# Performance work log

Hardware: AMD Instinct MI355X
Metric: run time of the kernel (lower is better)

The kernel has to match this reference:

```python
import jax, jax.numpy as jnp
import numpy as np

NP_, NA_ = 50000, 20000
D_IN, D_HID, D_OUT = 128, 128, 64
E_W, E_C, E_R = 250000, 500000, 250000


def setup_inputs() -> dict:
    key = jax.random.key(0)
    ks = jax.random.split(key, 14)
    s_in = 1.0 / np.sqrt(D_IN)
    s_h = 1.0 / np.sqrt(D_HID)
    return {
        "x_paper": jax.random.normal(ks[0], (NP_, D_IN), jnp.float32),
        "x_author": jax.random.normal(ks[1], (NA_, D_IN), jnp.float32),
        "Wl1": jax.random.normal(ks[2], (3, D_HID, D_IN), jnp.float32) * s_in,
        "bl1": jax.random.normal(ks[3], (3, D_HID), jnp.float32) * 0.01,
        "Wr1": jax.random.normal(ks[4], (3, D_HID, D_IN), jnp.float32) * s_in,
        "Wl2": jax.random.normal(ks[5], (3, D_OUT, D_HID), jnp.float32) * s_h,
        "bl2": jax.random.normal(ks[6], (3, D_OUT), jnp.float32) * 0.01,
        "Wr2": jax.random.normal(ks[7], (3, D_OUT, D_HID), jnp.float32) * s_h,
        "writes_src": jax.random.randint(ks[8], (E_W,), 0, NA_),
        "writes_dst": jax.random.randint(ks[9], (E_W,), 0, NP_),
        "cites_src": jax.random.randint(ks[10], (E_C,), 0, NP_),
        "cites_dst": jax.random.randint(ks[11], (E_C,), 0, NP_),
        "rev_src": jax.random.randint(ks[12], (E_R,), 0, NP_),
        "rev_dst": jax.random.randint(ks[13], (E_R,), 0, NA_),
    }


def _sage(x_src, x_dst, src, dst, Wl, bl, Wr, n_dst):
    # PyG SAGEConv(aggr='mean'): lin_l(mean_j x_src[j]) + lin_r(x_dst)
    agg = jax.ops.segment_sum(x_src[src], dst, num_segments=n_dst)
    cnt = jax.ops.segment_sum(jnp.ones_like(dst, dtype=x_src.dtype), dst,
                              num_segments=n_dst)
    agg = agg / jnp.maximum(cnt, 1.0)[:, None]  # degree-0 nodes -> 0 (PyG scatter-mean)
    return agg @ Wl.T + bl + x_dst @ Wr.T


def reference(x_paper, x_author, Wl1, bl1, Wr1, Wl2, bl2, Wr2,
              writes_src, writes_dst, cites_src, cites_dst, rev_src, rev_dst):
    def hetero_layer(xp, xa, Wl, bl, Wr):
        # HeteroConv(aggr='mean'): average per-relation outputs per dst node type
        op = 0.5 * (_sage(xa, xp, writes_src, writes_dst, Wl[0], bl[0], Wr[0], NP_)
                    + _sage(xp, xp, cites_src, cites_dst, Wl[1], bl[1], Wr[1], NP_))
        oa = _sage(xp, xa, rev_src, rev_dst, Wl[2], bl[2], Wr[2], NA_)
        return op, oa

    hp, ha = hetero_layer(x_paper, x_author, Wl1, bl1, Wr1)
    hp, ha = jax.nn.relu(hp), jax.nn.relu(ha)  # norm_type='none', dropout eval-mode
    hp, _ = hetero_layer(hp, ha, Wl2, bl2, Wr2)
    return hp  # logits for category='paper', [NP_, D_OUT]
```

## Files before the change

### kernel.cpp

```cpp
#include <hip/hip_runtime.h>

#define NP 50000
#define NA 20000
#define E_W 250000
#define E_C 500000
#define E_R 250000
#define E_TOT (E_W + E_C + E_R)
#define CAP 48
#define RBLK 8192
#define NSEG 123
#define NCHP 782
#define NCHA 313
#define NBIN (NCHP + NCHA)

typedef __attribute__((ext_vector_type(8))) short short8;
typedef __attribute__((ext_vector_type(4))) float floatx4;
typedef __attribute__((ext_vector_type(2))) float floatx2;

__device__ __forceinline__ unsigned short f2bf(float f) {
    unsigned u = __float_as_uint(f);
    return (unsigned short)((u + 0x7FFFu + ((u >> 16) & 1u)) >> 16);
}
__device__ __forceinline__ float bflo(unsigned v) { return __uint_as_float(v << 16); }
__device__ __forceinline__ float bfhi(unsigned v) { return __uint_as_float(v & 0xFFFF0000u); }

__device__ __forceinline__ int frag_off(int NT, int j, int n, int k) {
    int t = n >> 4, ln = n & 15;
    int kb = k >> 5, q = (k >> 3) & 3, r = k & 7;
    return (((j * NT + t) * 4 + kb) * 64 + q * 16 + ln) * 8 + r;
}

__device__ __forceinline__ void prep_body(
    int idx,
    const float* __restrict__ xp, const float* __restrict__ xa,
    const float* __restrict__ Wl1, const float* __restrict__ Wr1,
    const float* __restrict__ Wl2, const float* __restrict__ Wr2,
    const float* __restrict__ bl1, const float* __restrict__ bl2,
    unsigned short* __restrict__ xpb, unsigned short* __restrict__ xab,
    unsigned* __restrict__ xp8, unsigned* __restrict__ xa8,
    unsigned short* __restrict__ Wp1, unsigned short* __restrict__ Wa1,
    unsigned short* __restrict__ Wt2, unsigned short* __restrict__ Wr2s,
    float* __restrict__ bias_p1, float* __restrict__ bias_a1,
    float* __restrict__ bias_p2) {
    const int n4p = NP * 32, n4a = NA * 32;
    if (idx < n4p + n4a) {
        const float* s; unsigned short* d; unsigned* d8; int i = idx;
        if (i < n4p) { s = xp; d = xpb; d8 = xp8; }
        else { s = xa; d = xab; d8 = xa8; i -= n4p; }
        float4 v = ((const float4*)s)[i];
        ushort4 u;
        u.x = f2bf(v.x); u.y = f2bf(v.y); u.z = f2bf(v.z); u.w = f2bf(v.w);
        ((ushort4*)d)[i] = u;
        int w = __builtin_amdgcn_cvt_pk_fp8_f32(v.x, v.y, 0, false);
        w = __builtin_amdgcn_cvt_pk_fp8_f32(v.z, v.w, w, true);
        d8[i] = (unsigned)w;
        return;
    }
    int j = idx - (n4p + n4a);
    if (j < 49152) {
        int jj = j >> 14, rem = j & 16383, n = rem >> 7, k = rem & 127;
        float v = (jj == 0)   ? 0.5f * Wl1[rem]
                  : (jj == 1) ? 0.5f * Wl1[16384 + rem]
                              : 0.5f * (Wr1[rem] + Wr1[16384 + rem]);
        Wp1[frag_off(8, jj, n, k)] = f2bf(v);
    } else if (j < 81920) {
        int i2 = j - 49152;
        int jj = i2 >> 14, rem = i2 & 16383, n = rem >> 7, k = rem & 127;
        float v = (jj == 0) ? Wl1[2 * 16384 + rem] : Wr1[2 * 16384 + rem];
        Wa1[frag_off(8, jj, n, k)] = f2bf(v);
    } else if (j < 98304) {
        int i2 = j - 81920;
        int jj = i2 >> 13, rem = i2 & 8191, n = rem >> 7, k = rem & 127;
        float v = 0.5f * Wl2[jj * 8192 + rem];
        Wt2[frag_off(4, jj, n, k)] = f2bf(v);
    } else if (j < 106496) {
        int i2 = j - 98304;
        int n = i2 >> 7, k = i2 & 127;
        float v = 0.5f * (Wr2[i2] + Wr2[8192 + i2]);
        Wr2s[frag_off(4, 0, n, k)] = f2bf(v);
    } else if (j < 106496 + 320) {
        int b = j - 106496;
        if (b < 128) bias_p1[b] = 0.5f * (bl1[b] + bl1[128 + b]);
        else if (b < 256) bias_a1[b - 128] = bl1[256 + b - 128];
        else bias_p2[b - 256] = 0.5f * (bl2[b - 256] + bl2[64 + b - 256]);
    }
}

__device__ __forceinline__ void edge_bin(
    int e, const int* __restrict__ w_src, const int* __restrict__ w_dst,
    const int* __restrict__ c_src, const int* __restrict__ c_dst,
    const int* __restrict__ r_src, const int* __restrict__ r_dst,
    int& bin, int& sub, int& src) {
    bool isC = (e >= E_W) & (e < E_W + E_C);
    bool isR = e >= E_W + E_C;
    const int* db = isR ? r_dst : (isC ? c_dst : w_dst);
    const int* sb = isR ? r_src : (isC ? c_src : w_src);
    int idx = e - (isC ? E_W : 0) - (isR ? (E_W + E_C) : 0);
    int d = db[idx];
    src = sb[idx];
    if (isR) { bin = NCHP + (d >> 6); sub = d & 63; }
    else { bin = d >> 6; sub = (d & 63) + (isC ? 64 : 0); }
}

__device__ __forceinline__ void route_body(
    int bid, const int* __restrict__ w_src, const int* __restrict__ w_dst,
    const int* __restrict__ c_src, const int* __restrict__ c_dst,
    const int* __restrict__ r_src, const int* __restrict__ r_dst,
    unsigned* __restrict__ seg, unsigned* __restrict__ segmeta,
    int* cnt_s, int* base_s, int* cur_s) {
    int tid = threadIdx.x, lane = tid & 63;
    for (int k = tid; k < NBIN; k += 256) cnt_s[k] = 0;
    __syncthreads();
#pragma unroll 4
    for (int u = 0; u < 32; ++u) {
        int e = bid * RBLK + u * 256 + tid;
        if (e < E_TOT) {
            int bin, sub, src;
            edge_bin(e, w_src, w_dst, c_src, c_dst, r_src, r_dst, bin, sub, src);
            atomicAdd(&cnt_s[bin], 1);
        }
    }
    __syncthreads();
    if (tid < 64) {
        int v[18], tot = 0;
#pragma unroll
        for (int q = 0; q < 18; ++q) {
            int k = tid * 18 + q;
            v[q] = (k < NBIN) ? cnt_s[k] : 0;
            tot += v[q];
        }
        int sc = tot;
#pragma unroll
        for (int ofs = 1; ofs < 64; ofs <<= 1) {
            int t = __shfl_up(sc, ofs, 64);
            if (lane >= ofs) sc += t;
        }
        int run = sc - tot;
#pragma unroll
        for (int q = 0; q < 18; ++q) {
            int k = tid * 18 + q;
            if (k < NBIN) { base_s[k] = run; run += v[q]; }
        }
    }
    __syncthreads();
    for (int k = tid; k < NBIN; k += 256) {
        segmeta[bid * NBIN + k] = ((unsigned)base_s[k] << 16) | (unsigned)cnt_s[k];
        cur_s[k] = base_s[k];
    }
    __syncthreads();
    unsigned* segb = seg + (size_t)bid * RBLK;
#pragma unroll 4
    for (int u = 0; u < 32; ++u) {
        int e = bid * RBLK + u * 256 + tid;
        if (e < E_TOT) {
            int bin, sub, src;
            edge_bin(e, w_src, w_dst, c_src, c_dst, r_src, r_dst, bin, sub, src);
            int pos = atomicAdd(&cur_s[bin], 1);
            segb[pos] = (unsigned)src | ((unsigned)sub << 16);
        }
    }
}

__global__ __launch_bounds__(256) void route_prep(
    const float* xp, const float* xa, const float* Wl1, const float* Wr1,
    const float* Wl2, const float* Wr2, const float* bl1, const float* bl2,
    unsigned short* xpb, unsigned short* xab, unsigned* xp8, unsigned* xa8,
    unsigned short* Wp1, unsigned short* Wa1, unsigned short* Wt2, unsigned short* Wr2s,
    float* bias_p1, float* bias_a1, float* bias_p2,
    const int* w_src, const int* w_dst, const int* c_src, const int* c_dst,
    const int* r_src, const int* r_dst,
    unsigned* seg, unsigned* segmeta) {
    __shared__ int cnt_s[NBIN], base_s[NBIN], cur_s[NBIN];
    if ((int)blockIdx.x < NSEG)
        route_body(blockIdx.x, w_src, w_dst, c_src, c_dst, r_src, r_dst,
                   seg, segmeta, cnt_s, base_s, cur_s);
    else
        prep_body((blockIdx.x - NSEG) * 256 + threadIdx.x, xp, xa, Wl1, Wr1, Wl2, Wr2,
                  bl1, bl2, xpb, xab, xp8, xa8, Wp1, Wa1, Wt2, Wr2s,
                  bias_p1, bias_a1, bias_p2);
}

__global__ __launch_bounds__(512) void fill_l1(
    const unsigned* __restrict__ seg, const unsigned* __restrict__ segmeta,
    int* __restrict__ cnt, unsigned short* __restrict__ csr,
    const unsigned* __restrict__ xp8, const unsigned* __restrict__ xa8,
    const unsigned short* __restrict__ xpb, const unsigned short* __restrict__ xab,
    const unsigned short* __restrict__ Wp1, const float* __restrict__ bias_p1,
    const unsigned short* __restrict__ Wa1, const float* __restrict__ bias_a1,
    const unsigned short* __restrict__ Wt2, const unsigned short* __restrict__ Wr2s,
    unsigned short* __restrict__ ta, unsigned short* __restrict__ tp,
    float* __restrict__ sp) {
    __shared__ unsigned short rows[128 * CAP];
    __shared__ int cursor[128];
    __shared__ unsigned pkd[NSEG];
    __shared__ __align__(16) unsigned short aggL[128][136];
    int tid = threadIdx.x;
    int k = blockIdx.x;
    bool isPaper = k < NCHP;
    int base = isPaper ? k * 64 : (k - NCHP) * 64;
    int total = isPaper ? NP : NA;
    int M = total - base; if (M > 64) M = 64;

    for (int s = tid; s < NSEG; s += 512) pkd[s] = segmeta[s * NBIN + k];
    if (tid < 128) cursor[tid] = 0;
    __syncthreads();
    {
        int grp = tid >> 4, gl = tid & 15;
        for (int s = grp; s < NSEG; s += 32) {
            unsigned pk = pkd[s];
            int n = pk & 0xFFFFu;
            const unsigned* spq = seg + (size_t)s * RBLK + (pk >> 16);
            for (int i = gl; i < n; i += 16) {
                unsigned v = spq[i];
                int sub = v >> 16, srcn = v & 0xFFFFu;
                int pos = atomicAdd(&cursor[sub], 1);
                if (pos < CAP) rows[sub * CAP + pos] = (unsigned short)srcn;
            }
        }
    }
    __syncthreads();
    {
        const unsigned* s0 = isPaper ? xa8 : xp8;
        const unsigned* s1 = xp8;
        int d0 = isPaper ? NA : NP, d1 = NP;
        int LROWS = isPaper ? 128 : 64;
        int g = tid >> 5, sl = tid & 31;
        for (int l0 = g; l0 < LROWS; l0 += 32) {
            int lA = l0, lB = l0 + 16;
            const unsigned* sA = (lA & 64) ? s1 : s0;
            const unsigned* sB = (lB & 64) ? s1 : s0;
            int duA = (lA & 64) ? d1 : d0;
            int duB = (lB & 64) ? d1 : d0;
            int dA = cursor[lA], dB = cursor[lB];
            int cA = dA < CAP ? dA : CAP, cB = dB < CAP ? dB : CAP;
            int cm = cA > cB ? cA : cB;
            const unsigned short* rpA = &rows[lA * CAP];
            const unsigned short* rpB = &rows[lB * CAP];
            float a0 = 0.f, a1 = 0.f, a2 = 0.f, a3 = 0.f;
            float b0 = 0.f, b1 = 0.f, b2 = 0.f, b3 = 0.f;
            for (int i = 0; i < cm; i += 8) {
                short8 rA = *(const short8*)&rpA[i];
                short8 rB = *(const short8*)&rpB[i];
                unsigned vA[8], vB[8];
#pragma unroll
                for (int u = 0; u < 8; ++u) {
                    int q = (i + u < cA) ? (int)(unsigned short)rA[u] : duA;
                    vA[u] = sA[(q << 5) + sl];
                }
#pragma unroll
                for (int u = 0; u < 8; ++u) {
                    int q = (i + u < cB) ? (int)(unsigned short)rB[u] : duB;
                    vB[u] = sB[(q << 5) + sl];
                }
#pragma unroll
                for (int u = 0; u < 8; ++u) {
                    floatx2 lo = __builtin_amdgcn_cvt_pk_f32_fp8(vA[u], false);
                    floatx2 hi = __builtin_amdgcn_cvt_pk_f32_fp8(vA[u], true);
                    a0 += lo.x; a1 += lo.y; a2 += hi.x; a3 += hi.y;
                }
#pragma unroll
                for (int u = 0; u < 8; ++u) {
                    floatx2 lo = __builtin_amdgcn_cvt_pk_f32_fp8(vB[u], false);
                    floatx2 hi = __builtin_amdgcn_cvt_pk_f32_fp8(vB[u], true);
                    b0 += lo.x; b1 += lo.y; b2 += hi.x; b3 += hi.y;
                }
            }
            float sclA = dA > 0 ? 1.f / (float)dA : 0.f;
            float sclB = dB > 0 ? 1.f / (float)dB : 0.f;
            unsigned wloA = ((unsigned)f2bf(a1 * sclA) << 16) | (unsigned)f2bf(a0 * sclA);
            unsigned whiA = ((unsigned)f2bf(a3 * sclA) << 16) | (unsigned)f2bf(a2 * sclA);
            unsigned wloB = ((unsigned)f2bf(b1 * sclB) << 16) | (unsigned)f2bf(b0 * sclB);
            unsigned whiB = ((unsigned)f2bf(b3 * sclB) << 16) | (unsigned)f2bf(b2 * sclB);
            *(uint2*)&aggL[lA][sl * 4] = make_uint2(wloA, whiA);
            *(uint2*)&aggL[lB][sl * 4] = make_uint2(wloB, whiB);
        }
    }
    __syncthreads();
    int wave = tid >> 6, lane = tid & 63, ln = lane & 15, quad = lane >> 4;
    int wrow = (wave & 3) * 16, nhalf = wave >> 2;
    floatx4 acc[4];
#pragma unroll
    for (int t = 0; t < 4; ++t) acc[t] = (floatx4){0.f, 0.f, 0.f, 0.f};
    auto gemm_lds = [&](const unsigned short* __restrict__ Wb, int rowoff) {
#pragma unroll
        for (int kb = 0; kb < 4; ++kb) {
            short8 af = *(const short8*)&aggL[rowoff + wrow + ln][quad * 8 + kb * 32];
#pragma unroll
            for (int t = 0; t < 4; ++t) {
                short8 bf = *(const short8*)(Wb + ((nhalf * 4 + t) * 4 + kb) * 512 + lane * 8);
                acc[t] = __builtin_amdgcn_mfma_f32_16x16x32_bf16(af, bf, acc[t], 0, 0, 0);
            }
        }
    };
    auto gemm_glob = [&](const unsigned short* __restrict__ X,
                         const unsigned short* __restrict__ Wb) {
        int row = base + wrow + ln;
        int rowc = row < total ? row : total - 1;
        const unsigned short* A = X + (size_t)rowc * 128 + quad * 8;
#pragma unroll
        for (int kb = 0; kb < 4; ++kb) {
            short8 af = *(const short8*)(A + kb * 32);
#pragma unroll
            for (int t = 0; t < 4; ++t) {
                short8 bf = *(const short8*)(Wb + ((nhalf * 4 + t) * 4 + kb) * 512 + lane * 8);
                acc[t] = __builtin_amdgcn_mfma_f32_16x16x32_bf16(af, bf, acc[t], 0, 0, 0);
            }
        }
    };
    if (isPaper) {
        gemm_lds(Wp1, 0);
        gemm_lds(Wp1 + 16384, 64);
        gemm_glob(xpb, Wp1 + 2 * 16384);
    } else {
        gemm_lds(Wa1, 0);
        gemm_glob(xab, Wa1 + 16384);
    }
    __syncthreads();
    {
        const float* bias = isPaper ? bias_p1 : bias_a1;
#pragma unroll
        for (int t = 0; t < 4; ++t) {
            int col = nhalf * 64 + t * 16 + ln;
            float bv = bias[col];
#pragma unroll
            for (int r = 0; r < 4; ++r)
                aggL[wrow + quad * 4 + r][col] = f2bf(fmaxf(acc[t][r] + bv, 0.f));
        }
    }
    __syncthreads();
    floatx4 tacc[4];
#pragma unroll
    for (int t = 0; t < 4; ++t) tacc[t] = (floatx4){0.f, 0.f, 0.f, 0.f};
    int rows16 = (wave & 3) * 16;
    if (isPaper) {
        const unsigned short* W = (wave < 4) ? (Wt2 + 64 * 128) : Wr2s;
#pragma unroll
        for (int kb = 0; kb < 4; ++kb) {
            short8 af = *(const short8*)&aggL[rows16 + ln][quad * 8 + kb * 32];
#pragma unroll
            for (int t = 0; t < 4; ++t) {
                short8 bf = *(const short8*)(W + (t * 4 + kb) * 512 + lane * 8);
                tacc[t] = __builtin_amdgcn_mfma_f32_16x16x32_bf16(af, bf, tacc[t], 0, 0, 0);
            }
        }
#pragma unroll
        for (int t = 0; t < 4; ++t) {
            int col = t * 16 + ln;
#pragma unroll
            for (int r = 0; r < 4; ++r) {
                int lr = rows16 + quad * 4 + r;
                if (lr < M) {
                    if (wave < 4) tp[(size_t)(base + lr) * 64 + col] = f2bf(tacc[t][r]);
                    else sp[(size_t)(base + lr) * 64 + col] = tacc[t][r];
                }
            }
        }
    } else {
        int thalf = wave >> 2;
#pragma unroll
        for (int kb = 0; kb < 4; ++kb) {
            short8 af = *(const short8*)&aggL[rows16 + ln][quad * 8 + kb * 32];
#pragma unroll
            for (int tt = 0; tt < 2; ++tt) {
                short8 bf = *(const short8*)(Wt2 + ((thalf * 2 + tt) * 4 + kb) * 512 + lane * 8);
                tacc[tt] = __builtin_amdgcn_mfma_f32_16x16x32_bf16(af, bf, tacc[tt], 0, 0, 0);
            }
        }
#pragma unroll
        for (int tt = 0; tt < 2; ++tt) {
            int col = (thalf * 2 + tt) * 16 + ln;
#pragma unroll
            for (int r = 0; r < 4; ++r) {
                int lr = rows16 + quad * 4 + r;
                if (lr < M) ta[(size_t)(base + lr) * 64 + col] = f2bf(tacc[tt][r]);
            }
        }
    }
    if (isPaper) {
        for (int r = tid; r < 2 * M; r += 512)
            cnt[base * 2 + r] = cursor[(r >> 1) + ((r & 1) << 6)];
        const unsigned* rU = (const unsigned*)rows;
        unsigned* cU = (unsigned*)csr + (size_t)base * 2 * (CAP / 2);
        for (int i = tid; i < 2 * M * (CAP / 2); i += 512) {
            int r = i / (CAP / 2), j = i - r * (CAP / 2);
            cU[i] = rU[((r >> 1) + ((r & 1) << 6)) * (CAP / 2) + j];
        }
    }
}

__global__ void agg2(const unsigned short* __restrict__ ta, const unsigned short* __restrict__ tp,
                     const int* __restrict__ cnt, const unsigned short* __restrict__ csr,
                     const float* __restrict__ sp_in, const float* __restrict__ bias_p2,
                     float* __restrict__ out) {
    int node = blockIdx.x * 8 + (threadIdx.x >> 5);
    if (node >= NP) return;
    int lane = threadIdx.x & 63;
    int sl = lane & 31;
    int hw = lane & 32;
    float r0 = 0.f, r1 = 0.f;
#pragma unroll
    for (int rel = 0; rel < 2; ++rel) {
        int dummy = (rel == 0) ? NA : NP;
        const unsigned* sp = (const unsigned*)((rel == 0) ? ta : tp);
        int idx = node * 2 + rel;
        int deg = cnt[idx];
        int degc = deg < CAP ? deg : CAP;
        const unsigned short* row = csr + (size_t)idx * CAP;
        int ei0 = (sl < degc) ? (int)row[sl] : dummy;
        int ei1 = (32 + sl < degc) ? (int)row[32 + sl] : dummy;
        int degw = degc;
        int other = __shfl_xor(degw, 32, 64);
        if (other > degw) degw = other;
        float s0 = 0.f, s1 = 0.f, t0 = 0.f, t1 = 0.f;
        for (int i = 0; i < degw; i += 8) {
            unsigned v[8];
#pragma unroll
            for (int u = 0; u < 8; ++u) {
                int ii = i + u;
                int esrc = (ii < 32) ? ei0 : ei1;
                int qq = __shfl(esrc, hw | (ii & 31), 64);
                qq = (ii < degc) ? qq : dummy;
                v[u] = sp[(qq << 5) + sl];
            }
#pragma unroll
            for (int u = 0; u < 8; ++u) {
                if (u & 1) { t0 += bflo(v[u]); t1 += bfhi(v[u]); }
                else       { s0 += bflo(v[u]); s1 += bfhi(v[u]); }
            }
        }
        float scl = deg > 0 ? 1.f / (float)deg : 0.f;
        r0 += (s0 + t0) * scl; r1 += (s1 + t1) * scl;
    }
    float2 spv = ((const float2*)sp_in)[(size_t)node * 32 + sl];
    float2 bv = ((const float2*)bias_p2)[sl];
    ((float2*)out)[(size_t)node * 32 + sl] =
        make_float2(r0 + spv.x + bv.x, r1 + spv.y + bv.y);
}

extern "C" void kernel_launch(void* const* d_in, const int* in_sizes, int n_in,
                              void* d_out, int out_size, void* d_ws, size_t ws_size,
                              hipStream_t stream) {
    (void)in_sizes; (void)n_in; (void)out_size; (void)ws_size;
    const float* xp  = (const float*)d_in[0];
    const float* xa  = (const float*)d_in[1];
    const float* Wl1 = (const float*)d_in[2];
    const float* bl1 = (const float*)d_in[3];
    const float* Wr1 = (const float*)d_in[4];
    const float* Wl2 = (const float*)d_in[5];
    const float* bl2 = (const float*)d_in[6];
    const float* Wr2 = (const float*)d_in[7];
    const int* w_src = (const int*)d_in[8];
    const int* w_dst = (const int*)d_in[9];
    const int* c_src = (const int*)d_in[10];
    const int* c_dst = (const int*)d_in[11];
    const int* r_src = (const int*)d_in[12];
    const int* r_dst = (const int*)d_in[13];
    float* out = (float*)d_out;

    char* p = (char*)d_ws;
    auto alloc = [&](size_t bytes) {
        char* r = p;
        p += (bytes + 255) & ~(size_t)255;
        return r;
    };
    unsigned short* xpb   = (unsigned short*)alloc((size_t)NP * 128 * 2);
    unsigned short* xab   = (unsigned short*)alloc((size_t)NA * 128 * 2);
    unsigned*       xp8   = (unsigned*)alloc((size_t)(NP + 1) * 128);
    unsigned*       xa8   = (unsigned*)alloc((size_t)(NA + 1) * 128);
    unsigned short* ta    = (unsigned short*)alloc((size_t)(NA + 1) * 64 * 2);
    unsigned short* tp    = (unsigned short*)alloc((size_t)(NP + 1) * 64 * 2);
    float*          sp    = (float*)alloc((size_t)NP * 64 * 4);
    int*            cnt     = (int*)alloc((size_t)NP * 2 * 4);
    unsigned short* csr     = (unsigned short*)alloc((size_t)NP * 2 * CAP * 2);
    unsigned*       seg     = (unsigned*)alloc((size_t)NSEG * RBLK * 4);
    unsigned*       segmeta = (unsigned*)alloc((size_t)NSEG * NBIN * 4);
    unsigned short* Wp1  = (unsigned short*)alloc(3 * 128 * 128 * 2);
    unsigned short* Wa1  = (unsigned short*)alloc(2 * 128 * 128 * 2);
    unsigned short* Wt2  = (unsigned short*)alloc(2 * 64 * 128 * 2);
    unsigned short* Wr2s = (unsigned short*)alloc(64 * 128 * 2);
    float* bias_p1 = (float*)alloc(128 * 4);
    float* bias_a1 = (float*)alloc(128 * 4);
    float* bias_p2 = (float*)alloc(64 * 4);

    hipMemsetAsync(xp8 + (size_t)NP * 32, 0, 128, stream);
    hipMemsetAsync(xa8 + (size_t)NA * 32, 0, 128, stream);
    hipMemsetAsync(ta + (size_t)NA * 64, 0, 128, stream);
    hipMemsetAsync(tp + (size_t)NP * 64, 0, 128, stream);

    int prep_threads = (NP + NA) * 32 + 106496 + 320;
    int prep_blocks = (prep_threads + 255) / 256;
    route_prep<<<NSEG + prep_blocks, 256, 0, stream>>>(
        xp, xa, Wl1, Wr1, Wl2, Wr2, bl1, bl2,
        xpb, xab, xp8, xa8, Wp1, Wa1, Wt2, Wr2s, bias_p1, bias_a1, bias_p2,
        w_src, w_dst, c_src, c_dst, r_src, r_dst, seg, segmeta);

    fill_l1<<<NBIN, 512, 0, stream>>>(seg, segmeta, cnt, csr,
                                      xp8, xa8, xpb, xab, Wp1, bias_p1, Wa1, bias_a1,
                                      Wt2, Wr2s, ta, tp, sp);

    agg2<<<(NP + 7) / 8, 256, 0, stream>>>(ta, tp, cnt, csr, sp, bias_p2, out);
}
```

Baseline: 204.0 us.

## Interleave both relations' gathers in agg2 and widen route_prep blocks to 512

agg2 now walks the writes and cites neighbor lists in one fused loop, issuing both relations' gather loads together so more memory requests are in flight per wavefront. route_prep moves from 256 to 512 threads per block, so each route block covers its 8192-edge segment in 16 iterations instead of 32. The prep part is relaunched with half as many blocks. The fused agg2 loop runs to the larger of the two degrees, which adds padded dummy loads for the shorter list and raises register use.

```diff
diff --git a/kernel.cpp b/kernel.cpp
--- a/kernel.cpp
+++ b/kernel.cpp
@@ -109,11 +109,11 @@
     unsigned* __restrict__ seg, unsigned* __restrict__ segmeta,
     int* cnt_s, int* base_s, int* cur_s) {
     int tid = threadIdx.x, lane = tid & 63;
-    for (int k = tid; k < NBIN; k += 256) cnt_s[k] = 0;
+    for (int k = tid; k < NBIN; k += 512) cnt_s[k] = 0;
     __syncthreads();
 #pragma unroll 4
-    for (int u = 0; u < 32; ++u) {
-        int e = bid * RBLK + u * 256 + tid;
+    for (int u = 0; u < 16; ++u) {
+        int e = bid * RBLK + u * 512 + tid;
         if (e < E_TOT) {
             int bin, sub, src;
             edge_bin(e, w_src, w_dst, c_src, c_dst, r_src, r_dst, bin, sub, src);
@@ -143,15 +143,15 @@
         }
     }
     __syncthreads();
-    for (int k = tid; k < NBIN; k += 256) {
+    for (int k = tid; k < NBIN; k += 512) {
         segmeta[bid * NBIN + k] = ((unsigned)base_s[k] << 16) | (unsigned)cnt_s[k];
         cur_s[k] = base_s[k];
     }
     __syncthreads();
     unsigned* segb = seg + (size_t)bid * RBLK;
 #pragma unroll 4
-    for (int u = 0; u < 32; ++u) {
-        int e = bid * RBLK + u * 256 + tid;
+    for (int u = 0; u < 16; ++u) {
+        int e = bid * RBLK + u * 512 + tid;
         if (e < E_TOT) {
             int bin, sub, src;
             edge_bin(e, w_src, w_dst, c_src, c_dst, r_src, r_dst, bin, sub, src);
@@ -161,7 +161,7 @@
     }
 }
 
-__global__ __launch_bounds__(256) void route_prep(
+__global__ __launch_bounds__(512) void route_prep(
     const float* xp, const float* xa, const float* Wl1, const float* Wr1,
     const float* Wl2, const float* Wr2, const float* bl1, const float* bl2,
     unsigned short* xpb, unsigned short* xab, unsigned* xp8, unsigned* xa8,
@@ -175,7 +175,7 @@
         route_body(blockIdx.x, w_src, w_dst, c_src, c_dst, r_src, r_dst,
                    seg, segmeta, cnt_s, base_s, cur_s);
     else
-        prep_body((blockIdx.x - NSEG) * 256 + threadIdx.x, xp, xa, Wl1, Wr1, Wl2, Wr2,
+        prep_body((blockIdx.x - NSEG) * 512 + threadIdx.x, xp, xa, Wl1, Wr1, Wl2, Wr2,
                   bl1, bl2, xpb, xab, xp8, xa8, Wp1, Wa1, Wt2, Wr2s,
                   bias_p1, bias_a1, bias_p2);
 }
@@ -397,40 +397,55 @@
     int lane = threadIdx.x & 63;
     int sl = lane & 31;
     int hw = lane & 32;
-    float r0 = 0.f, r1 = 0.f;
-#pragma unroll
-    for (int rel = 0; rel < 2; ++rel) {
-        int dummy = (rel == 0) ? NA : NP;
-        const unsigned* sp = (const unsigned*)((rel == 0) ? ta : tp);
-        int idx = node * 2 + rel;
-        int deg = cnt[idx];
-        int degc = deg < CAP ? deg : CAP;
-        const unsigned short* row = csr + (size_t)idx * CAP;
-        int ei0 = (sl < degc) ? (int)row[sl] : dummy;
-        int ei1 = (32 + sl < degc) ? (int)row[32 + sl] : dummy;
-        int degw = degc;
-        int other = __shfl_xor(degw, 32, 64);
-        if (other > degw) degw = other;
-        float s0 = 0.f, s1 = 0.f, t0 = 0.f, t1 = 0.f;
-        for (int i = 0; i < degw; i += 8) {
-            unsigned v[8];
-#pragma unroll
-            for (int u = 0; u < 8; ++u) {
-                int ii = i + u;
-                int esrc = (ii < 32) ? ei0 : ei1;
-                int qq = __shfl(esrc, hw | (ii & 31), 64);
-                qq = (ii < degc) ? qq : dummy;
-                v[u] = sp[(qq << 5) + sl];
-            }
-#pragma unroll
-            for (int u = 0; u < 8; ++u) {
-                if (u & 1) { t0 += bflo(v[u]); t1 += bfhi(v[u]); }
-                else       { s0 += bflo(v[u]); s1 += bfhi(v[u]); }
-            }
-        }
-        float scl = deg > 0 ? 1.f / (float)deg : 0.f;
-        r0 += (s0 + t0) * scl; r1 += (s1 + t1) * scl;
-    }
+    const unsigned* t0p = (const unsigned*)ta;
+    const unsigned* t1p = (const unsigned*)tp;
+    int deg0 = cnt[node * 2], deg1 = cnt[node * 2 + 1];
+    int c0 = deg0 < CAP ? deg0 : CAP;
+    int c1 = deg1 < CAP ? deg1 : CAP;
+    const unsigned short* row0 = csr + (size_t)node * 2 * CAP;
+    const unsigned short* row1 = row0 + CAP;
+    int e00 = (sl < c0) ? (int)row0[sl] : NA;
+    int e01 = (32 + sl < c0) ? (int)row0[32 + sl] : NA;
+    int e10 = (sl < c1) ? (int)row1[sl] : NP;
+    int e11 = (32 + sl < c1) ? (int)row1[32 + sl] : NP;
+    int degw = c0 > c1 ? c0 : c1;
+    int other = __shfl_xor(degw, 32, 64);
+    if (other > degw) degw = other;
+    float sa0 = 0.f, sa1 = 0.f, sb0 = 0.f, sb1 = 0.f;
+    float ua0 = 0.f, ua1 = 0.f, ub0 = 0.f, ub1 = 0.f;
+    for (int i = 0; i < degw; i += 8) {
+        unsigned v0[8], v1[8];
+#pragma unroll
+        for (int u = 0; u < 8; ++u) {
+            int ii = i + u;
+            int es = (ii < 32) ? e00 : e01;
+            int qq = __shfl(es, hw | (ii & 31), 64);
+            qq = (ii < c0) ? qq : NA;
+            v0[u] = t0p[(qq << 5) + sl];
+        }
+#pragma unroll
+        for (int u = 0; u < 8; ++u) {
+            int ii = i + u;
+            int es = (ii < 32) ? e10 : e11;
+            int qq = __shfl(es, hw | (ii & 31), 64);
+            qq = (ii < c1) ? qq : NP;
+            v1[u] = t1p[(qq << 5) + sl];
+        }
+#pragma unroll
+        for (int u = 0; u < 8; ++u) {
+            if (u & 1) { sb0 += bflo(v0[u]); sb1 += bfhi(v0[u]); }
+            else       { sa0 += bflo(v0[u]); sa1 += bfhi(v0[u]); }
+        }
+#pragma unroll
+        for (int u = 0; u < 8; ++u) {
+            if (u & 1) { ub0 += bflo(v1[u]); ub1 += bfhi(v1[u]); }
+            else       { ua0 += bflo(v1[u]); ua1 += bfhi(v1[u]); }
+        }
+    }
+    float scl0 = deg0 > 0 ? 1.f / (float)deg0 : 0.f;
+    float scl1 = deg1 > 0 ? 1.f / (float)deg1 : 0.f;
+    float r0 = (sa0 + sb0) * scl0 + (ua0 + ub0) * scl1;
+    float r1 = (sa1 + sb1) * scl0 + (ua1 + ub1) * scl1;
     float2 spv = ((const float2*)sp_in)[(size_t)node * 32 + sl];
     float2 bv = ((const float2*)bias_p2)[sl];
     ((float2*)out)[(size_t)node * 32 + sl] =
@@ -488,8 +503,8 @@
     hipMemsetAsync(tp + (size_t)NP * 64, 0, 128, stream);
 
     int prep_threads = (NP + NA) * 32 + 106496 + 320;
-    int prep_blocks = (prep_threads + 255) / 256;
-    route_prep<<<NSEG + prep_blocks, 256, 0, stream>>>(
+    int prep_blocks = (prep_threads + 511) / 512;
+    route_prep<<<NSEG + prep_blocks, 512, 0, stream>>>(
         xp, xa, Wl1, Wr1, Wl2, Wr2, bl1, bl2,
         xpb, xab, xp8, xa8, Wp1, Wa1, Wt2, Wr2s, bias_p1, bias_a1, bias_p2,
         w_src, w_dst, c_src, c_dst, r_src, r_dst, seg, segmeta);
```

After: 199.5 us. 1.02x faster.
